# Kernel tuning notes

Hardware: AMD Instinct MI355X
Metric: run time of the kernel (lower is better)

The kernel has to match this reference:

```python
import jax, jax.numpy as jnp
import numpy as np

D_MODEL = 1024
NUM_HEADS = 16
D_K = D_MODEL // NUM_HEADS


def setup_inputs() -> dict:
    key = jax.random.key(0)
    ks = jax.random.split(key, 11)
    B, T = 4, 2048
    s = 1.0 / np.sqrt(D_MODEL)
    inp = {
        "query": jax.random.normal(ks[0], (B, T, D_MODEL), jnp.float32),
        "key": jax.random.normal(ks[1], (B, T, D_MODEL), jnp.float32),
        "value": jax.random.normal(ks[2], (B, T, D_MODEL), jnp.float32),
        "Wq": jax.random.uniform(ks[3], (D_MODEL, D_MODEL), jnp.float32, -s, s),
        "bq": jax.random.uniform(ks[4], (D_MODEL,), jnp.float32, -s, s),
        "Wk": jax.random.uniform(ks[5], (D_MODEL, D_MODEL), jnp.float32, -s, s),
        "bk": jax.random.uniform(ks[6], (D_MODEL,), jnp.float32, -s, s),
        "Wv": jax.random.uniform(ks[7], (D_MODEL, D_MODEL), jnp.float32, -s, s),
        "bv": jax.random.uniform(ks[8], (D_MODEL,), jnp.float32, -s, s),
        "Wo": jax.random.uniform(ks[9], (D_MODEL, D_MODEL), jnp.float32, -s, s),
        "bo": jax.random.uniform(ks[10], (D_MODEL,), jnp.float32, -s, s),
    }
    return inp


def _split_heads(x):
    B, T, _ = x.shape
    return x.reshape(B, T, NUM_HEADS, D_K).transpose(0, 2, 1, 3)  # (B,H,T,dk)


def reference(query, key, value, Wq, bq, Wk, bk, Wv, bv, Wo, bo):
    q = _split_heads(query @ Wq + bq)   # (B,H,Tq,dk)
    k = _split_heads(key @ Wk + bk)     # (B,H,Tk,dk)
    v = _split_heads(value @ Wv + bv)   # (B,H,Tk,dk)
    scale = 1.0 / jnp.sqrt(jnp.asarray(D_K, q.dtype))
    scores = jnp.einsum("bhqd,bhkd->bhqk", q, k) * scale
    weights = jax.nn.softmax(scores, axis=-1)
    attn = jnp.einsum("bhqk,bhkd->bhqd", weights, v)  # (B,H,Tq,dk)
    B, H, T, dk = attn.shape
    attn = attn.transpose(0, 2, 1, 3).reshape(B, T, H * dk)
    return attn @ Wo + bo
```

## Files before the change

### kernel.cpp

```cpp
#include <hip/hip_runtime.h>
#include <hip/hip_bf16.h>
#include <stdint.h>


typedef __bf16 bf16x8 __attribute__((ext_vector_type(8)));
typedef short  v4s    __attribute__((ext_vector_type(4)));
typedef float  f32x4  __attribute__((ext_vector_type(4)));

#define LOG2E 1.44269504088896340736f

static __device__ __forceinline__ uint32_t f2bf(float x) {
  uint32_t u = __float_as_uint(x);
  u += 0x7fffu + ((u >> 16) & 1u);
  return u >> 16;
}
#if __has_builtin(__builtin_amdgcn_cvt_pk_bf16_f32)
static __device__ __forceinline__ uint32_t pk2bf(float a, float b) {
  typedef __bf16 b2 __attribute__((ext_vector_type(2)));
  union { b2 v; uint32_t u; } x;
  x.v = __builtin_amdgcn_cvt_pk_bf16_f32(a, b);
  return x.u;
}
#else
static __device__ __forceinline__ uint32_t pk2bf(float a, float b) {
  return f2bf(a) | (f2bf(b) << 16);
}
#endif
static __device__ __forceinline__ void gl2lds16(const void* g, void* l) {
  __builtin_amdgcn_global_load_lds(
      (const __attribute__((address_space(1))) uint32_t*)g,
      (__attribute__((address_space(3))) uint32_t*)l, 16, 0, 0);
}

__global__ void convert_inputs(const float* __restrict__ q, const float* __restrict__ k,
                               const float* __restrict__ v, uint16_t* __restrict__ qo,
                               uint16_t* __restrict__ ko, uint16_t* __restrict__ vo) {
  const float* src = blockIdx.y == 0 ? q : (blockIdx.y == 1 ? k : v);
  uint16_t*    dst = blockIdx.y == 0 ? qo : (blockIdx.y == 1 ? ko : vo);
  size_t idx = ((size_t)blockIdx.x * 256 + threadIdx.x) * 8;
  float4 a = *(const float4*)(src + idx);
  float4 b = *(const float4*)(src + idx + 4);
  uint4 o;
  o.x = pk2bf(a.x, a.y); o.y = pk2bf(a.z, a.w);
  o.z = pk2bf(b.x, b.y); o.w = pk2bf(b.z, b.w);
  *(uint4*)(dst + idx) = o;
}

__global__ void transpose_weights(const float* __restrict__ Wq, const float* __restrict__ Wk,
                                  const float* __restrict__ Wv, const float* __restrict__ Wo,
                                  uint16_t* __restrict__ out) {
  __shared__ float t[32][33];
  const float* W = blockIdx.z == 0 ? Wq : blockIdx.z == 1 ? Wk : blockIdx.z == 2 ? Wv : Wo;
  uint16_t* O = out + (size_t)blockIdx.z * 1048576;
  int tx = threadIdx.x & 31, ty = threadIdx.x >> 5;
  int r0 = blockIdx.y * 32, c0 = blockIdx.x * 32;
#pragma unroll
  for (int i = 0; i < 4; i++) t[ty + i * 8][tx] = W[(size_t)(r0 + ty + i * 8) * 1024 + c0 + tx];
  __syncthreads();
#pragma unroll
  for (int i = 0; i < 4; i++)
    O[(size_t)(c0 + ty + i * 8) * 1024 + r0 + tx] = (uint16_t)f2bf(t[tx][ty + i * 8]);
}

static __device__ __forceinline__ void gemm_body(
    const uint16_t* __restrict__ A, const uint16_t* __restrict__ Bt,
    const float* __restrict__ bias, void* __restrict__ Cout,
    int N, int K, int mode, float oscale, int mBase, int nBase,
    uint16_t* __restrict__ lA, uint16_t* __restrict__ lB) {
  int tid = threadIdx.x, wave = tid >> 6, lane = tid & 63;
  int q = lane >> 4, c = lane & 15;
  int wrow = wave & 1, wcol = wave >> 1;
  f32x4 acc[4][4] = {};

  int swz = ((lane & 7) ^ (lane >> 3)) * 8;
  const uint16_t* gA = A + (size_t)(mBase + wave * 32 + (lane >> 3)) * K + swz;
  const uint16_t* gB = Bt + (size_t)(nBase + wave * 32 + (lane >> 3)) * K + swz;
  int cs = c & 7;

  for (int kt = 0; kt < K / 64; kt++) {
    __syncthreads();
    int k0 = kt * 64;
#pragma unroll
    for (int it = 0; it < 4; it++) {
      gl2lds16(gA + (size_t)(it * 8) * K + k0, &lA[(wave * 32 + it * 8) * 64]);
      gl2lds16(gB + (size_t)(it * 8) * K + k0, &lB[(wave * 32 + it * 8) * 64]);
    }
    __syncthreads();
#pragma unroll
    for (int kk = 0; kk < 2; kk++) {
      bf16x8 af[4], bfr[4];
#pragma unroll
      for (int i = 0; i < 4; i++)
        af[i] = *(const bf16x8*)&lA[(wrow * 64 + i * 16 + c) * 64 + ((kk * 4 + q) ^ cs) * 8];
#pragma unroll
      for (int j = 0; j < 4; j++)
        bfr[j] = *(const bf16x8*)&lB[(wcol * 64 + j * 16 + c) * 64 + ((kk * 4 + q) ^ cs) * 8];
#pragma unroll
      for (int i = 0; i < 4; i++)
#pragma unroll
        for (int j = 0; j < 4; j++)
          acc[i][j] = __builtin_amdgcn_mfma_f32_16x16x32_bf16(af[i], bfr[j], acc[i][j], 0, 0, 0);
    }
  }

  float bb[4];
#pragma unroll
  for (int j = 0; j < 4; j++) bb[j] = bias[nBase + wcol * 64 + j * 16 + c];

  if (mode == 0) {
    float* Co = (float*)Cout;
#pragma unroll
    for (int i = 0; i < 4; i++)
#pragma unroll
      for (int j = 0; j < 4; j++) {
        int row = mBase + wrow * 64 + i * 16 + q * 4;
        int col = nBase + wcol * 64 + j * 16 + c;
#pragma unroll
        for (int r = 0; r < 4; r++) Co[(size_t)(row + r) * N + col] = acc[i][j][r] + bb[j];
      }
  } else if (mode == 1) {
    uint16_t* Co = (uint16_t*)Cout;
#pragma unroll
    for (int i = 0; i < 4; i++)
#pragma unroll
      for (int j = 0; j < 4; j++) {
        int row = mBase + wrow * 64 + i * 16 + q * 4;
        int col = nBase + wcol * 64 + j * 16 + c;
#pragma unroll
        for (int r = 0; r < 4; r++)
          Co[(size_t)(row + r) * N + col] = (uint16_t)f2bf((acc[i][j][r] + bb[j]) * oscale);
      }
  } else {
    uint16_t* Co = (uint16_t*)Cout;
#pragma unroll
    for (int i = 0; i < 4; i++)
#pragma unroll
      for (int j = 0; j < 4; j++) {
        int n = nBase + wcol * 64 + j * 16 + c;
        int h = n >> 6, d = n & 63;
        int m = mBase + wrow * 64 + i * 16 + q * 4;
        int b = m >> 11, t = m & 2047;
        uint32_t lo = pk2bf(acc[i][j][0] + bb[j], acc[i][j][1] + bb[j]);
        uint32_t hi = pk2bf(acc[i][j][2] + bb[j], acc[i][j][3] + bb[j]);
        *(uint2*)(Co + (size_t)((b * 16 + h) * 64 + d) * 2048 + t) = make_uint2(lo, hi);
      }
  }
}

__global__ __launch_bounds__(256, 2)
void gemm_qkv(const uint16_t* __restrict__ qb, const uint16_t* __restrict__ kb,
              const uint16_t* __restrict__ vb, const uint16_t* __restrict__ Wtq,
              const uint16_t* __restrict__ Wtk, const uint16_t* __restrict__ Wtv,
              const float* __restrict__ bq, const float* __restrict__ bk,
              const float* __restrict__ bv, uint16_t* __restrict__ Qp,
              uint16_t* __restrict__ Kp, uint16_t* __restrict__ Vt, float cs) {
  __shared__ uint16_t lA[8192], lB[8192];
  int z = blockIdx.z;
  const uint16_t* A  = z == 0 ? qb : (z == 1 ? kb : vb);
  const uint16_t* Bt = z == 0 ? Wtq : (z == 1 ? Wtk : Wtv);
  const float* bias  = z == 0 ? bq : (z == 1 ? bk : bv);
  void* C            = z == 0 ? (void*)Qp : (z == 1 ? (void*)Kp : (void*)Vt);
  int mode   = z == 2 ? 2 : 1;
  float os   = z == 0 ? cs : 1.0f;
  gemm_body(A, Bt, bias, C, 1024, 1024, mode, os, blockIdx.y * 128, blockIdx.x * 128, lA, lB);
}

__global__ __launch_bounds__(256, 2)
void gemm_out(const uint16_t* __restrict__ A, const uint16_t* __restrict__ Bt,
              const float* __restrict__ bias, float* __restrict__ C) {
  __shared__ uint16_t lA[8192], lB[8192];
  gemm_body(A, Bt, bias, C, 1024, 1024, 0, 1.0f, blockIdx.y * 128, blockIdx.x * 128, lA, lB);
}

__global__ __launch_bounds__(256, 2)
void attn(const uint16_t* __restrict__ Qp, const uint16_t* __restrict__ Kp,
          const uint16_t* __restrict__ Vt, uint16_t* __restrict__ Ob) {
  __shared__ uint16_t lds[16384];
  int tid = threadIdx.x, wave = tid >> 6, lane = tid & 63;
  int q = lane >> 4, c = lane & 15;
  int cs = c & 7;

  int id = blockIdx.y * 16 + blockIdx.x;
  int wk = (id & 7) * 128 + (id >> 3);
  int qt = wk & 15, bh = wk >> 4;
  int b = bh >> 4, h = bh & 15;
  int qbase = qt * 128;
  int swz = ((lane & 7) ^ (lane >> 3)) * 8;

  {
    const uint16_t* gQ =
        Qp + (size_t)(b * 2048 + qbase + wave * 32 + (lane >> 3)) * 1024 + h * 64 + swz;
#pragma unroll
    for (int it = 0; it < 4; it++)
      gl2lds16(gQ + (size_t)(it * 8) * 1024, &lds[(wave * 32 + it * 8) * 64]);
  }
  __syncthreads();
  bf16x8 qf[2][2];
#pragma unroll
  for (int it = 0; it < 2; it++)
#pragma unroll
    for (int kk = 0; kk < 2; kk++)
      qf[it][kk] =
          *(const bf16x8*)&lds[(wave * 32 + it * 16 + c) * 64 + ((kk * 4 + q) ^ cs) * 8];
  __syncthreads();

  f32x4 o[4][2] = {};
  float rs0 = 0.f, rs1 = 0.f;

  const uint16_t* gK0 =
      Kp + (size_t)(b * 2048 + wave * 16 + (lane >> 3)) * 1024 + h * 64 + swz;
  const uint16_t* gV0 = Vt + (size_t)(bh * 64 + wave * 16 + (lane >> 3)) * 2048 + swz;

#pragma unroll
  for (int it = 0; it < 2; it++) {
    gl2lds16(gK0 + (size_t)(it * 8) * 1024, &lds[(wave * 16 + it * 8) * 64]);
    gl2lds16(gV0 + (size_t)(it * 8) * 2048, &lds[8192 + (wave * 16 + it * 8) * 64]);
  }

  for (int kt = 0; kt < 32; kt++) {
    int cur = kt & 1;
    __syncthreads();

    if (kt < 31) {
      int nb = (cur ^ 1) * 4096;
#pragma unroll
      for (int it = 0; it < 2; it++) {
        gl2lds16(gK0 + (size_t)((kt + 1) * 64 + it * 8) * 1024,
                 &lds[nb + (wave * 16 + it * 8) * 64]);
        gl2lds16(gV0 + (size_t)(it * 8) * 2048 + (kt + 1) * 64,
                 &lds[8192 + nb + (wave * 16 + it * 8) * 64]);
      }
    }

    const uint16_t* sKc = &lds[cur * 4096];
    const uint16_t* sVc = &lds[8192 + cur * 4096];

#pragma unroll
    for (int jt = 0; jt < 4; jt++) {
      bf16x8 a0 = *(const bf16x8*)&sKc[(jt * 16 + c) * 64 + (q ^ cs) * 8];
      bf16x8 a1 = *(const bf16x8*)&sKc[(jt * 16 + c) * 64 + ((4 + q) ^ cs) * 8];
      f32x4 s0 = __builtin_amdgcn_mfma_f32_16x16x32_bf16(a0, qf[0][0],
                                                         (f32x4){0.f, 0.f, 0.f, 0.f}, 0, 0, 0);
      s0 = __builtin_amdgcn_mfma_f32_16x16x32_bf16(a1, qf[0][1], s0, 0, 0, 0);
      f32x4 s1 = __builtin_amdgcn_mfma_f32_16x16x32_bf16(a0, qf[1][0],
                                                         (f32x4){0.f, 0.f, 0.f, 0.f}, 0, 0, 0);
      s1 = __builtin_amdgcn_mfma_f32_16x16x32_bf16(a1, qf[1][1], s1, 0, 0, 0);

      float p00 = __builtin_amdgcn_exp2f(s0[0]), p01 = __builtin_amdgcn_exp2f(s0[1]);
      float p02 = __builtin_amdgcn_exp2f(s0[2]), p03 = __builtin_amdgcn_exp2f(s0[3]);
      float p10 = __builtin_amdgcn_exp2f(s1[0]), p11 = __builtin_amdgcn_exp2f(s1[1]);
      float p12 = __builtin_amdgcn_exp2f(s1[2]), p13 = __builtin_amdgcn_exp2f(s1[3]);
      rs0 += (p00 + p01) + (p02 + p03);
      rs1 += (p10 + p11) + (p12 + p13);
      union { uint32_t u[2]; v4s s4; } pb0, pb1;
      pb0.u[0] = pk2bf(p00, p01); pb0.u[1] = pk2bf(p02, p03);
      pb1.u[0] = pk2bf(p10, p11); pb1.u[1] = pk2bf(p12, p13);

#pragma unroll
      for (int mt = 0; mt < 4; mt++) {
        v4s a = *(const v4s*)&sVc[(mt * 16 + c) * 64 + (((jt * 2 + (q >> 1)) ^ cs) * 8) +
                                  (q & 1) * 4];
        o[mt][0] = __builtin_amdgcn_mfma_f32_16x16x16bf16_1k(a, pb0.s4, o[mt][0], 0, 0, 0);
        o[mt][1] = __builtin_amdgcn_mfma_f32_16x16x16bf16_1k(a, pb1.s4, o[mt][1], 0, 0, 0);
      }
    }
  }

  rs0 += __shfl_xor(rs0, 16); rs0 += __shfl_xor(rs0, 32);
  rs1 += __shfl_xor(rs1, 16); rs1 += __shfl_xor(rs1, 32);
  float l[2] = {rs0, rs1};

#pragma unroll
  for (int it = 0; it < 2; it++) {
    float inv = 1.0f / l[it];
    size_t trow = (size_t)(b * 2048 + qbase + wave * 32 + it * 16 + c) * 1024 + h * 64;
#pragma unroll
    for (int mt = 0; mt < 4; mt++) {
      uint32_t lo = pk2bf(o[mt][it][0] * inv, o[mt][it][1] * inv);
      uint32_t hi = pk2bf(o[mt][it][2] * inv, o[mt][it][3] * inv);
      *(uint2*)(Ob + trow + mt * 16 + q * 4) = make_uint2(lo, hi);
    }
  }
}

extern "C" void kernel_launch(void* const* d_in, const int* in_sizes, int n_in,
                              void* d_out, int out_size, void* d_ws, size_t ws_size,
                              hipStream_t stream) {
  (void)in_sizes; (void)n_in; (void)out_size; (void)ws_size;
  const float* query = (const float*)d_in[0];
  const float* key_  = (const float*)d_in[1];
  const float* value = (const float*)d_in[2];
  const float* Wq = (const float*)d_in[3]; const float* bq = (const float*)d_in[4];
  const float* Wk = (const float*)d_in[5]; const float* bk = (const float*)d_in[6];
  const float* Wv = (const float*)d_in[7]; const float* bv = (const float*)d_in[8];
  const float* Wo = (const float*)d_in[9]; const float* bo = (const float*)d_in[10];

  const size_t SZ = (size_t)8192 * 1024;
  uint16_t* buf0 = (uint16_t*)d_ws;
  uint16_t* buf1 = buf0 + SZ;
  uint16_t* buf2 = buf1 + SZ;
  uint16_t* buf3 = buf2 + SZ;
  uint16_t* wts  = buf3 + SZ;
  uint16_t* Wtq = wts;
  uint16_t* Wtk = wts + 1048576;
  uint16_t* Wtv = wts + 2097152;
  uint16_t* Wto = wts + 3145728;
  uint16_t* Kp  = wts + 4194304;
  uint16_t* Vt  = Kp + SZ;

  const float Cs = 0.125f * LOG2E;

  convert_inputs<<<dim3(4096, 3), 256, 0, stream>>>(query, key_, value, buf0, buf1, buf2);
  transpose_weights<<<dim3(32, 32, 4), 256, 0, stream>>>(Wq, Wk, Wv, Wo, wts);
  gemm_qkv<<<dim3(8, 64, 3), 256, 0, stream>>>(buf0, buf1, buf2, Wtq, Wtk, Wtv,
                                               bq, bk, bv, buf3, Kp, Vt, Cs);
  attn<<<dim3(16, 64), 256, 0, stream>>>(buf3, Kp, Vt, buf2);
  gemm_out<<<dim3(8, 64), 256, 0, stream>>>(buf2, Wto, bo, (float*)d_out);
}
```

Measured before the change: 355.1 us.

## Remap GEMM blocks per XCD, software-pipeline QK MFMAs, compute rowsum via MFMA

```diff
diff --git a/kernel.cpp b/kernel.cpp
--- a/kernel.cpp
+++ b/kernel.cpp
@@ -155,21 +155,29 @@
               const float* __restrict__ bv, uint16_t* __restrict__ Qp,
               uint16_t* __restrict__ Kp, uint16_t* __restrict__ Vt, float cs) {
   __shared__ uint16_t lA[8192], lB[8192];
-  int z = blockIdx.z;
+  int id = blockIdx.x + (blockIdx.y << 3) + (blockIdx.z << 9);
+  int xcd = id & 7, j = id >> 3;
+  int by = xcd * 8 + (j & 7);
+  int bx = (j >> 3) & 7;
+  int z  = j >> 6;
   const uint16_t* A  = z == 0 ? qb : (z == 1 ? kb : vb);
   const uint16_t* Bt = z == 0 ? Wtq : (z == 1 ? Wtk : Wtv);
   const float* bias  = z == 0 ? bq : (z == 1 ? bk : bv);
   void* C            = z == 0 ? (void*)Qp : (z == 1 ? (void*)Kp : (void*)Vt);
   int mode   = z == 2 ? 2 : 1;
   float os   = z == 0 ? cs : 1.0f;
-  gemm_body(A, Bt, bias, C, 1024, 1024, mode, os, blockIdx.y * 128, blockIdx.x * 128, lA, lB);
+  gemm_body(A, Bt, bias, C, 1024, 1024, mode, os, by * 128, bx * 128, lA, lB);
 }
 
 __global__ __launch_bounds__(256, 2)
 void gemm_out(const uint16_t* __restrict__ A, const uint16_t* __restrict__ Bt,
               const float* __restrict__ bias, float* __restrict__ C) {
   __shared__ uint16_t lA[8192], lB[8192];
-  gemm_body(A, Bt, bias, C, 1024, 1024, 0, 1.0f, blockIdx.y * 128, blockIdx.x * 128, lA, lB);
+  int id = blockIdx.x + (blockIdx.y << 3);
+  int xcd = id & 7, j = id >> 3;
+  int by = xcd * 8 + (j & 7);
+  int bx = j >> 3;
+  gemm_body(A, Bt, bias, C, 1024, 1024, 0, 1.0f, by * 128, bx * 128, lA, lB);
 }
 
 __global__ __launch_bounds__(256, 2)
@@ -205,7 +213,8 @@
   __syncthreads();
 
   f32x4 o[4][2] = {};
-  float rs0 = 0.f, rs1 = 0.f;
+  f32x4 lacc[2] = {};
+  const v4s vone = {(short)0x3F80, (short)0x3F80, (short)0x3F80, (short)0x3F80};
 
   const uint16_t* gK0 =
       Kp + (size_t)(b * 2048 + wave * 16 + (lane >> 3)) * 1024 + h * 64 + swz;
@@ -235,26 +244,40 @@
     const uint16_t* sKc = &lds[cur * 4096];
     const uint16_t* sVc = &lds[8192 + cur * 4096];
 
+    f32x4 s0, s1, n0, n1;
+    {
+      bf16x8 a0 = *(const bf16x8*)&sKc[(c)*64 + (q ^ cs) * 8];
+      bf16x8 a1 = *(const bf16x8*)&sKc[(c)*64 + ((4 + q) ^ cs) * 8];
+      s0 = __builtin_amdgcn_mfma_f32_16x16x32_bf16(a0, qf[0][0],
+                                                   (f32x4){0.f, 0.f, 0.f, 0.f}, 0, 0, 0);
+      s0 = __builtin_amdgcn_mfma_f32_16x16x32_bf16(a1, qf[0][1], s0, 0, 0, 0);
+      s1 = __builtin_amdgcn_mfma_f32_16x16x32_bf16(a0, qf[1][0],
+                                                   (f32x4){0.f, 0.f, 0.f, 0.f}, 0, 0, 0);
+      s1 = __builtin_amdgcn_mfma_f32_16x16x32_bf16(a1, qf[1][1], s1, 0, 0, 0);
+    }
 #pragma unroll
     for (int jt = 0; jt < 4; jt++) {
-      bf16x8 a0 = *(const bf16x8*)&sKc[(jt * 16 + c) * 64 + (q ^ cs) * 8];
-      bf16x8 a1 = *(const bf16x8*)&sKc[(jt * 16 + c) * 64 + ((4 + q) ^ cs) * 8];
-      f32x4 s0 = __builtin_amdgcn_mfma_f32_16x16x32_bf16(a0, qf[0][0],
-                                                         (f32x4){0.f, 0.f, 0.f, 0.f}, 0, 0, 0);
-      s0 = __builtin_amdgcn_mfma_f32_16x16x32_bf16(a1, qf[0][1], s0, 0, 0, 0);
-      f32x4 s1 = __builtin_amdgcn_mfma_f32_16x16x32_bf16(a0, qf[1][0],
-                                                         (f32x4){0.f, 0.f, 0.f, 0.f}, 0, 0, 0);
-      s1 = __builtin_amdgcn_mfma_f32_16x16x32_bf16(a1, qf[1][1], s1, 0, 0, 0);
+      if (jt < 3) {
+        bf16x8 a0 = *(const bf16x8*)&sKc[((jt + 1) * 16 + c) * 64 + (q ^ cs) * 8];
+        bf16x8 a1 = *(const bf16x8*)&sKc[((jt + 1) * 16 + c) * 64 + ((4 + q) ^ cs) * 8];
+        n0 = __builtin_amdgcn_mfma_f32_16x16x32_bf16(a0, qf[0][0],
+                                                     (f32x4){0.f, 0.f, 0.f, 0.f}, 0, 0, 0);
+        n0 = __builtin_amdgcn_mfma_f32_16x16x32_bf16(a1, qf[0][1], n0, 0, 0, 0);
+        n1 = __builtin_amdgcn_mfma_f32_16x16x32_bf16(a0, qf[1][0],
+                                                     (f32x4){0.f, 0.f, 0.f, 0.f}, 0, 0, 0);
+        n1 = __builtin_amdgcn_mfma_f32_16x16x32_bf16(a1, qf[1][1], n1, 0, 0, 0);
+      }
 
       float p00 = __builtin_amdgcn_exp2f(s0[0]), p01 = __builtin_amdgcn_exp2f(s0[1]);
       float p02 = __builtin_amdgcn_exp2f(s0[2]), p03 = __builtin_amdgcn_exp2f(s0[3]);
       float p10 = __builtin_amdgcn_exp2f(s1[0]), p11 = __builtin_amdgcn_exp2f(s1[1]);
       float p12 = __builtin_amdgcn_exp2f(s1[2]), p13 = __builtin_amdgcn_exp2f(s1[3]);
-      rs0 += (p00 + p01) + (p02 + p03);
-      rs1 += (p10 + p11) + (p12 + p13);
       union { uint32_t u[2]; v4s s4; } pb0, pb1;
       pb0.u[0] = pk2bf(p00, p01); pb0.u[1] = pk2bf(p02, p03);
       pb1.u[0] = pk2bf(p10, p11); pb1.u[1] = pk2bf(p12, p13);
+
+      lacc[0] = __builtin_amdgcn_mfma_f32_16x16x16bf16_1k(vone, pb0.s4, lacc[0], 0, 0, 0);
+      lacc[1] = __builtin_amdgcn_mfma_f32_16x16x16bf16_1k(vone, pb1.s4, lacc[1], 0, 0, 0);
 
 #pragma unroll
       for (int mt = 0; mt < 4; mt++) {
@@ -263,12 +286,11 @@
         o[mt][0] = __builtin_amdgcn_mfma_f32_16x16x16bf16_1k(a, pb0.s4, o[mt][0], 0, 0, 0);
         o[mt][1] = __builtin_amdgcn_mfma_f32_16x16x16bf16_1k(a, pb1.s4, o[mt][1], 0, 0, 0);
       }
-    }
-  }
-
-  rs0 += __shfl_xor(rs0, 16); rs0 += __shfl_xor(rs0, 32);
-  rs1 += __shfl_xor(rs1, 16); rs1 += __shfl_xor(rs1, 32);
-  float l[2] = {rs0, rs1};
+      if (jt < 3) { s0 = n0; s1 = n1; }
+    }
+  }
+
+  float l[2] = {lacc[0][0], lacc[1][0]};
 
 #pragma unroll
   for (int it = 0; it < 2; it++) {
```

Result: no change. 348.2 us (-1.9%).
